# Performance work log

Hardware: AMD Instinct MI355X
Metric: run time of the kernel (lower is better)

Reference implementation:

```python
import jax, jax.numpy as jnp
import numpy as np

B, S = 2, 2048
NUM_HEADS, NUM_KV_HEADS, HEAD_DIM = 32, 8, 128
HIDDEN = NUM_HEADS * HEAD_DIM  # 4096
Q_SIZE = NUM_HEADS * HEAD_DIM
KV_SIZE = NUM_KV_HEADS * HEAD_DIM
ROPE_THETA = 100000.0
SCALE = HEAD_DIM ** -0.5


def setup_inputs() -> dict:
    key = jax.random.key(0)
    k1, k2, k3, k4, k5 = jax.random.split(key, 5)
    T = B * S
    return {
        "hidden_states": jax.random.normal(k1, (T, HIDDEN), jnp.float32) * 0.02,
        "positions": jnp.arange(T, dtype=jnp.int64) % S,  # per-sequence positions
        "w_qkv": jax.random.normal(k2, (HIDDEN, Q_SIZE + 2 * KV_SIZE), jnp.float32) * 0.02,
        "b_qkv": jax.random.normal(k3, (Q_SIZE + 2 * KV_SIZE,), jnp.float32) * 0.01,
        "w_o": jax.random.normal(k4, (Q_SIZE, HIDDEN), jnp.float32) * 0.02,
        "b_o": jax.random.normal(k5, (HIDDEN,), jnp.float32) * 0.01,
    }


def _rope_neox(x, positions):
    # x: [T, H, D]; neox style rotates the two halves of head_dim
    half = HEAD_DIM // 2
    inv_freq = 1.0 / (ROPE_THETA ** (jnp.arange(0, HEAD_DIM, 2, dtype=jnp.float32) / HEAD_DIM))
    freqs = positions.astype(jnp.float32)[:, None] * inv_freq[None, :]  # [T, D/2]
    cos = jnp.cos(freqs)[:, None, :]  # [T, 1, D/2]
    sin = jnp.sin(freqs)[:, None, :]
    x1, x2 = x[..., :half], x[..., half:]
    return jnp.concatenate([x1 * cos - x2 * sin, x2 * cos + x1 * sin], axis=-1)


def reference(hidden_states, positions, w_qkv, b_qkv, w_o, b_o):
    T = hidden_states.shape[0]
    qkv = hidden_states @ w_qkv + b_qkv  # [T, q+2kv]
    q = qkv[:, :Q_SIZE].reshape(T, NUM_HEADS, HEAD_DIM)
    k = qkv[:, Q_SIZE:Q_SIZE + KV_SIZE].reshape(T, NUM_KV_HEADS, HEAD_DIM)
    v = qkv[:, Q_SIZE + KV_SIZE:].reshape(T, NUM_KV_HEADS, HEAD_DIM)

    q = _rope_neox(q, positions)
    k = _rope_neox(k, positions)

    # reshape flattened tokens back to [B, S, ...] for causal self-attention
    q = q.reshape(B, S, NUM_HEADS, HEAD_DIM)
    k = k.reshape(B, S, NUM_KV_HEADS, HEAD_DIM)
    v = v.reshape(B, S, NUM_KV_HEADS, HEAD_DIM)

    # GQA: repeat kv heads to match query heads
    group = NUM_HEADS // NUM_KV_HEADS
    k = jnp.repeat(k, group, axis=2)  # [B, S, H, D]
    v = jnp.repeat(v, group, axis=2)

    scores = jnp.einsum("bqhd,bkhd->bhqk", q, k) * SCALE  # [B, H, S, S]
    causal = jnp.tril(jnp.ones((S, S), dtype=bool))
    scores = jnp.where(causal[None, None], scores, jnp.finfo(scores.dtype).min)
    probs = jax.nn.softmax(scores, axis=-1)
    attn = jnp.einsum("bhqk,bkhd->bqhd", probs, v)  # [B, S, H, D]

    attn = attn.reshape(T, Q_SIZE)
    return attn @ w_o + b_o  # [T, HIDDEN]
```

## Files before the change

### kernel.cpp

```cpp
#include <hip/hip_runtime.h>
#include <cstdint>
#include <math.h>

#define T_TOTAL 4096
#define S_LEN   2048
#define NH      32
#define NKV     8
#define HD      128
#define HIDDEN  4096
#define QSZ     4096
#define KVSZ    1024
#define QKV_N   6144
#define SCALE_F 0.08838834764831843f

typedef __bf16 bf16x8 __attribute__((ext_vector_type(8)));
typedef float  f32x4  __attribute__((ext_vector_type(4)));
typedef unsigned short u16;
typedef unsigned int   u32;
typedef u16 u16x8 __attribute__((ext_vector_type(8)));
typedef u16 u16x4 __attribute__((ext_vector_type(4)));

__device__ __forceinline__ u16 f2bf(float f) {
  u32 b = __float_as_uint(f);
  b += 0x7FFFu + ((b >> 16) & 1u);
  return (u16)(b >> 16);
}

__device__ __forceinline__ void async_copy16(const u16* g, u16* l) {
  __builtin_amdgcn_global_load_lds(
      (const __attribute__((address_space(1))) void*)(g),
      (__attribute__((address_space(3))) void*)(l), 16, 0, 0);
}

__global__ __launch_bounds__(256) void cast_bf16_kernel(const float4* __restrict__ in,
                                                        ushort4* __restrict__ out, int n4) {
  int i = blockIdx.x * 256 + threadIdx.x;
  if (i >= n4) return;
  float4 v = in[i];
  ushort4 o;
  o.x = f2bf(v.x); o.y = f2bf(v.y); o.z = f2bf(v.z); o.w = f2bf(v.w);
  out[i] = o;
}

__global__ __launch_bounds__(256) void transpose_cast_kernel(const float* __restrict__ in,
                                                             u16* __restrict__ out, int R, int C) {
  __shared__ float tile[32][33];
  int bx = blockIdx.x * 32;
  int by = blockIdx.y * 32;
  int tx = threadIdx.x & 31, ty = threadIdx.x >> 5;
  for (int i = ty; i < 32; i += 8)
    tile[i][tx] = in[(size_t)(by + i) * C + bx + tx];
  __syncthreads();
  for (int i = ty; i < 32; i += 8)
    out[(size_t)(bx + i) * R + by + tx] = f2bf(tile[tx][i]);
}

__global__ __launch_bounds__(256) void gemm_bt_kernel(const u16* __restrict__ A,
                                                      const u16* __restrict__ Bt,
                                                      const float* __restrict__ bias,
                                                      float* __restrict__ C,
                                                      int M, int N, int K) {
  __shared__ u16 sA[128 * 32];
  __shared__ u16 sB[128 * 32];
  const int tid  = threadIdx.x;
  const int lane = tid & 63, wave = tid >> 6;
  const int quad = lane >> 4, l16 = lane & 15;
  const int wm = (wave >> 1) * 64, wn = (wave & 1) * 64;
  const int bm = blockIdx.y, bn = blockIdx.x;

  const u16* gA0 = A  + (size_t)(bm * 128 + (tid >> 2)) * K + (tid & 3) * 8;
  const u16* gA1 = gA0 + (size_t)64 * K;
  const u16* gB0 = Bt + (size_t)(bn * 128 + (tid >> 2)) * K + (tid & 3) * 8;
  const u16* gB1 = gB0 + (size_t)64 * K;
  u16* lA0 = &sA[(size_t)tid * 8];
  u16* lA1 = &sA[(size_t)(256 + tid) * 8];
  u16* lB0 = &sB[(size_t)tid * 8];
  u16* lB1 = &sB[(size_t)(256 + tid) * 8];

  f32x4 acc[4][4] = {};

  for (int kt = 0; kt < K; kt += 32) {
    __syncthreads();
    async_copy16(gA0 + kt, lA0);
    async_copy16(gA1 + kt, lA1);
    async_copy16(gB0 + kt, lB0);
    async_copy16(gB1 + kt, lB1);
    __syncthreads();

    bf16x8 af[4], bfr[4];
#pragma unroll
    for (int i = 0; i < 4; ++i)
      af[i] = *(const bf16x8*)&sA[(wm + i * 16 + l16) * 32 + quad * 8];
#pragma unroll
    for (int j = 0; j < 4; ++j)
      bfr[j] = *(const bf16x8*)&sB[(wn + j * 16 + l16) * 32 + quad * 8];
#pragma unroll
    for (int i = 0; i < 4; ++i)
#pragma unroll
      for (int j = 0; j < 4; ++j)
        acc[i][j] = __builtin_amdgcn_mfma_f32_16x16x32_bf16(af[i], bfr[j], acc[i][j], 0, 0, 0);
  }

#pragma unroll
  for (int i = 0; i < 4; ++i) {
    int row0 = bm * 128 + wm + i * 16 + quad * 4;
#pragma unroll
    for (int j = 0; j < 4; ++j) {
      int col = bn * 128 + wn + j * 16 + l16;
      float bi = bias[col];
#pragma unroll
      for (int r = 0; r < 4; ++r)
        C[(size_t)(row0 + r) * N + col] = acc[i][j][r] + bi;
    }
  }
}

__global__ __launch_bounds__(256) void qk_rope_cast_kernel(const float* __restrict__ qkv,
                                                           const int* __restrict__ pos,
                                                           u16* __restrict__ Qb,
                                                           u16* __restrict__ Kb) {
  int idx = blockIdx.x * 256 + threadIdx.x;
  int t = idx / 2560;
  int rem = idx - t * 2560;
  int head = rem >> 6, i = rem & 63;
  int b = t >> 11, s = t & 2047;
  float p = (float)pos[t];
  float inv = exp2f(-(float)i * 0.25952563f);
  float f = p * inv;
  float sn, cs;
  sincosf(f, &sn, &cs);
  if (head < NH) {
    const float* src = qkv + (size_t)t * QKV_N + head * HD;
    float x1 = src[i], x2 = src[i + 64];
    u16* dst = Qb + (((size_t)(b * NH + head)) * S_LEN + s) * HD;
    dst[i]      = f2bf((x1 * cs - x2 * sn) * SCALE_F);
    dst[i + 64] = f2bf((x2 * cs + x1 * sn) * SCALE_F);
  } else {
    int kh = head - NH;
    const float* src = qkv + (size_t)t * QKV_N + QSZ + kh * HD;
    float x1 = src[i], x2 = src[i + 64];
    u16* dst = Kb + (((size_t)(b * NKV + kh)) * S_LEN + s) * HD;
    dst[i]      = f2bf(x1 * cs - x2 * sn);
    dst[i + 64] = f2bf(x2 * cs + x1 * sn);
  }
}

__global__ __launch_bounds__(256) void v_transpose_cast_kernel(const float* __restrict__ qkv,
                                                               u16* __restrict__ Vtb) {
  __shared__ float tile[32][33];
  int st = blockIdx.x * 32;
  int dt = blockIdx.y * 32;
  int bk = blockIdx.z;
  int b = bk >> 3, kvh = bk & 7;
  int tx = threadIdx.x & 31, ty = threadIdx.x >> 5;
  const float* src = qkv + (size_t)(b * S_LEN) * QKV_N + QSZ + KVSZ + kvh * HD;
  for (int i = ty; i < 32; i += 8)
    tile[i][tx] = src[(size_t)(st + i) * QKV_N + dt + tx];
  __syncthreads();
  u16* dst = Vtb + (size_t)bk * HD * S_LEN;
  for (int i = ty; i < 32; i += 8)
    dst[(size_t)(dt + i) * S_LEN + st + tx] = f2bf(tile[tx][i]);
}

__global__ __launch_bounds__(256) void flash_mfma_kernel(const u16* __restrict__ Qb,
                                                         const u16* __restrict__ Kb,
                                                         const u16* __restrict__ Vtb,
                                                         u16* __restrict__ attn) {
  const int qti = gridDim.x - 1 - blockIdx.x;
  const int h = blockIdx.y, b = blockIdx.z;
  const int kvh = h >> 2;
  const int tid = threadIdx.x;
  const int lane = tid & 63, wave = tid >> 6;
  const int quad = lane >> 4, l16 = lane & 15;

  __shared__ u16 sK[64 * 128];
  __shared__ u16 sVt[128 * 64];
  __shared__ u16 sP[4][16 * 64];

  bf16x8 qf[4];
  {
    const u16* qrow = Qb + (((size_t)(b * NH + h)) * S_LEN + (size_t)qti * 64 + wave * 16 + l16) * HD;
#pragma unroll
    for (int kc = 0; kc < 4; ++kc)
      qf[kc] = *(const bf16x8*)(qrow + kc * 32 + quad * 8);
  }

  f32x4 acc[8] = {};
  float m_r = -INFINITY;
  float l_r = 0.f;

  const u16* Kbase = Kb  + ((size_t)(b * NKV + kvh)) * S_LEN * HD;
  const u16* Vbase = Vtb + ((size_t)(b * NKV + kvh)) * HD * S_LEN;

  u16x8 kv[4], vv[4];
#pragma unroll
  for (int i = 0; i < 4; ++i) {
    int c = i * 256 + tid;
    kv[i] = *(const u16x8*)(Kbase + (size_t)(c >> 4) * HD + (c & 15) * 8);
    vv[i] = *(const u16x8*)(Vbase + (size_t)(c >> 3) * S_LEN + (c & 7) * 8);
  }

  for (int kt = 0; kt <= qti; ++kt) {
    __syncthreads();
#pragma unroll
    for (int i = 0; i < 4; ++i) {
      int c = i * 256 + tid;
      int kr = c >> 4;
      *(u16x8*)&sK[(kr * 128 + (c & 15) * 8) ^ ((kr & 7) << 3)] = kv[i];
      int vr = c >> 3;
      *(u16x8*)&sVt[(vr * 64 + (c & 7) * 8) ^ ((vr & 7) << 3)] = vv[i];
    }
    __syncthreads();

    if (kt < qti) {
#pragma unroll
      for (int i = 0; i < 4; ++i) {
        int c = i * 256 + tid;
        kv[i] = *(const u16x8*)(Kbase + (size_t)((kt + 1) * 64 + (c >> 4)) * HD + (c & 15) * 8);
        vv[i] = *(const u16x8*)(Vbase + (size_t)(c >> 3) * S_LEN + (kt + 1) * 64 + (c & 7) * 8);
      }
    }

    f32x4 s[4] = {};
#pragma unroll
    for (int kc = 0; kc < 4; ++kc) {
#pragma unroll
      for (int nb = 0; nb < 4; ++nb) {
        bf16x8 kf = *(const bf16x8*)&sK[((nb * 16 + l16) * 128 + kc * 32 + quad * 8) ^ ((l16 & 7) << 3)];
        s[nb] = __builtin_amdgcn_mfma_f32_16x16x32_bf16(kf, qf[kc], s[nb], 0, 0, 0);
      }
    }

    if (kt == qti) {
      int qloc = wave * 16 + l16;
#pragma unroll
      for (int nb = 0; nb < 4; ++nb)
#pragma unroll
        for (int r = 0; r < 4; ++r)
          if (nb * 16 + quad * 4 + r > qloc) s[nb][r] = -1e30f;
    }

    float mx = -1e30f;
#pragma unroll
    for (int nb = 0; nb < 4; ++nb)
#pragma unroll
      for (int r = 0; r < 4; ++r)
        mx = fmaxf(mx, s[nb][r]);
    mx = fmaxf(mx, __shfl_xor(mx, 16));
    mx = fmaxf(mx, __shfl_xor(mx, 32));
    float mnew = fmaxf(m_r, mx);
    float alpha = __expf(m_r - mnew);
    m_r = mnew;
    float rs = 0.f;
#pragma unroll
    for (int nb = 0; nb < 4; ++nb)
#pragma unroll
      for (int r = 0; r < 4; ++r) {
        float p = __expf(s[nb][r] - mnew);
        s[nb][r] = p;
        rs += p;
      }
    rs += __shfl_xor(rs, 16);
    rs += __shfl_xor(rs, 32);
    l_r = l_r * alpha + rs;

#pragma unroll
    for (int db = 0; db < 8; ++db)
#pragma unroll
      for (int r = 0; r < 4; ++r)
        acc[db][r] *= alpha;

    u16* sPw = sP[wave];
#pragma unroll
    for (int nb = 0; nb < 4; ++nb) {
      u16x4 pk;
#pragma unroll
      for (int r = 0; r < 4; ++r) pk[r] = f2bf(s[nb][r]);
      *(u16x4*)&sPw[(l16 * 64 + nb * 16 + quad * 4) ^ ((l16 & 7) << 3)] = pk;
    }

#pragma unroll
    for (int ch = 0; ch < 2; ++ch) {
      bf16x8 pf = *(const bf16x8*)&sPw[(l16 * 64 + ch * 32 + quad * 8) ^ ((l16 & 7) << 3)];
#pragma unroll
      for (int db = 0; db < 8; ++db) {
        bf16x8 vf = *(const bf16x8*)&sVt[((db * 16 + l16) * 64 + ch * 32 + quad * 8) ^ ((l16 & 7) << 3)];
        acc[db] = __builtin_amdgcn_mfma_f32_16x16x32_bf16(vf, pf, acc[db], 0, 0, 0);
      }
    }
  }

  float invl = 1.0f / l_r;
  __syncthreads();
  u16* sOw = &sK[wave * 2048];
#pragma unroll
  for (int db = 0; db < 8; ++db) {
    u16x4 pk;
#pragma unroll
    for (int r = 0; r < 4; ++r) pk[r] = f2bf(acc[db][r] * invl);
    *(u16x4*)&sOw[(l16 * 128 + db * 16 + quad * 4) ^ ((l16 & 7) << 3)] = pk;
  }
#pragma unroll
  for (int p = 0; p < 4; ++p) {
    int row = p * 4 + quad;
    u16x8 o = *(const u16x8*)&sOw[(row * 128 + l16 * 8) ^ ((row & 7) << 3)];
    int q = qti * 64 + wave * 16 + row;
    *(u16x8*)(attn + ((size_t)(b * S_LEN + q)) * QSZ + (size_t)h * HD + l16 * 8) = o;
  }
}

extern "C" void kernel_launch(void* const* d_in, const int* in_sizes, int n_in,
                              void* d_out, int out_size, void* d_ws, size_t ws_size,
                              hipStream_t stream) {
  const float* hidden    = (const float*)d_in[0];
  const int*   positions = (const int*)d_in[1];
  const float* w_qkv     = (const float*)d_in[2];
  const float* b_qkv     = (const float*)d_in[3];
  const float* w_o       = (const float*)d_in[4];
  const float* b_o       = (const float*)d_in[5];
  float* out = (float*)d_out;

  char* ws = (char*)d_ws;
  const size_t MB = 1024 * 1024;
  u16*   hb    = (u16*)ws;
  u16*   wqT   = (u16*)(ws + 32  * MB);
  u16*   woT   = (u16*)(ws + 80  * MB);
  float* qkv   = (float*)(ws + 112 * MB);
  u16*   attnb = (u16*)(ws + 208 * MB);
  u16*   Qb    = (u16*)ws;
  u16*   Kb    = (u16*)(ws + 32 * MB);
  u16*   Vtb   = (u16*)(ws + 40 * MB);

  cast_bf16_kernel<<<T_TOTAL * HIDDEN / 4 / 256, 256, 0, stream>>>(
      (const float4*)hidden, (ushort4*)hb, T_TOTAL * HIDDEN / 4);
  transpose_cast_kernel<<<dim3(QKV_N / 32, HIDDEN / 32), 256, 0, stream>>>(w_qkv, wqT, HIDDEN, QKV_N);
  transpose_cast_kernel<<<dim3(HIDDEN / 32, QSZ / 32), 256, 0, stream>>>(w_o, woT, QSZ, HIDDEN);
  gemm_bt_kernel<<<dim3(QKV_N / 128, T_TOTAL / 128), 256, 0, stream>>>(
      hb, wqT, b_qkv, qkv, T_TOTAL, QKV_N, HIDDEN);
  qk_rope_cast_kernel<<<T_TOTAL * 2560 / 256, 256, 0, stream>>>(qkv, positions, Qb, Kb);
  v_transpose_cast_kernel<<<dim3(S_LEN / 32, HD / 32, 16), 256, 0, stream>>>(qkv, Vtb);
  flash_mfma_kernel<<<dim3(S_LEN / 64, NH, 2), 256, 0, stream>>>(Qb, Kb, Vtb, attnb);
  gemm_bt_kernel<<<dim3(HIDDEN / 128, T_TOTAL / 128), 256, 0, stream>>>(
      attnb, woT, b_o, out, T_TOTAL, HIDDEN, QSZ);
}
```

Baseline: 1.020 ms.

## Replace GEMM with triple-buffered 256x256 tile kernel with swizzled LDS and XCD remap

Both projection GEMMs now use a new kernel with 512 threads and 256x256 output tiles. It keeps three stages of async global-to-LDS copies in flight with explicit vmcnt waits, so loads overlap the MFMA work. LDS columns are XOR-swizzled to cut bank conflicts, and block IDs are remapped across the 8 XCDs to improve L2 locality. The larger tiles and 3x32KB of LDS reduce occupancy, and fewer blocks (384 and 256) means less parallelism to fill the machine.

```diff
diff --git a/kernel.cpp b/kernel.cpp
--- a/kernel.cpp
+++ b/kernel.cpp
@@ -55,58 +55,82 @@
     out[(size_t)(bx + i) * R + by + tx] = f2bf(tile[tx][i]);
 }
 
-__global__ __launch_bounds__(256) void gemm_bt_kernel(const u16* __restrict__ A,
-                                                      const u16* __restrict__ Bt,
-                                                      const float* __restrict__ bias,
-                                                      float* __restrict__ C,
-                                                      int M, int N, int K) {
-  __shared__ u16 sA[128 * 32];
-  __shared__ u16 sB[128 * 32];
+__global__ __launch_bounds__(512) void gemm_pipe_kernel(const u16* __restrict__ A,
+                                                        const u16* __restrict__ Bt,
+                                                        const float* __restrict__ bias,
+                                                        float* __restrict__ C,
+                                                        int M, int N, int K, int nbn) {
+  __shared__ u16 lds[3][2][8192];
   const int tid  = threadIdx.x;
   const int lane = tid & 63, wave = tid >> 6;
   const int quad = lane >> 4, l16 = lane & 15;
-  const int wm = (wave >> 1) * 64, wn = (wave & 1) * 64;
-  const int bm = blockIdx.y, bn = blockIdx.x;
-
-  const u16* gA0 = A  + (size_t)(bm * 128 + (tid >> 2)) * K + (tid & 3) * 8;
-  const u16* gA1 = gA0 + (size_t)64 * K;
-  const u16* gB0 = Bt + (size_t)(bn * 128 + (tid >> 2)) * K + (tid & 3) * 8;
-  const u16* gB1 = gB0 + (size_t)64 * K;
-  u16* lA0 = &sA[(size_t)tid * 8];
-  u16* lA1 = &sA[(size_t)(256 + tid) * 8];
-  u16* lB0 = &sB[(size_t)tid * 8];
-  u16* lB1 = &sB[(size_t)(256 + tid) * 8];
-
-  f32x4 acc[4][4] = {};
-
-  for (int kt = 0; kt < K; kt += 32) {
-    __syncthreads();
-    async_copy16(gA0 + kt, lA0);
-    async_copy16(gA1 + kt, lA1);
-    async_copy16(gB0 + kt, lB0);
-    async_copy16(gB1 + kt, lB1);
-    __syncthreads();
-
-    bf16x8 af[4], bfr[4];
-#pragma unroll
-    for (int i = 0; i < 4; ++i)
-      af[i] = *(const bf16x8*)&sA[(wm + i * 16 + l16) * 32 + quad * 8];
+  const int wm = (wave >> 2) * 128;
+  const int wn = (wave & 3) * 64;
+
+  const int cpx = gridDim.x >> 3;
+  const int logical = (blockIdx.x & 7) * cpx + (blockIdx.x >> 3);
+  const int bm = logical / nbn, bn = logical % nbn;
+
+  const int trow = tid >> 2;
+  const int gch  = ((tid & 3) ^ ((tid >> 3) & 3)) * 8;
+  const u16* gA = A  + (size_t)(bm * 256 + trow) * K + gch;
+  const u16* gB = Bt + (size_t)(bn * 256 + trow) * K + gch;
+  const size_t eoff = (size_t)128 * K;
+
+  const int NT = K >> 5;
+#pragma unroll
+  for (int pt = 0; pt < 3; ++pt) {
+    int kt = pt * 32;
+    async_copy16(gA + kt,        &lds[pt][0][tid * 8]);
+    async_copy16(gA + eoff + kt, &lds[pt][0][4096 + tid * 8]);
+    async_copy16(gB + kt,        &lds[pt][1][tid * 8]);
+    async_copy16(gB + eoff + kt, &lds[pt][1][4096 + tid * 8]);
+  }
+
+  const int sw = (quad ^ ((l16 >> 1) & 3)) * 8;
+  f32x4 acc[8][4] = {};
+  int sl = 0;
+  for (int t = 0; t < NT; ++t) {
+    int rem = NT - t;
+    if (rem >= 3)      asm volatile("s_waitcnt vmcnt(8)" ::: "memory");
+    else if (rem == 2) asm volatile("s_waitcnt vmcnt(4)" ::: "memory");
+    else               asm volatile("s_waitcnt vmcnt(0)" ::: "memory");
+    __builtin_amdgcn_s_barrier();
+
+    const u16* sAt = lds[sl][0];
+    const u16* sBt = lds[sl][1];
+    bf16x8 af[8], bfr[4];
+#pragma unroll
+    for (int i = 0; i < 8; ++i)
+      af[i] = *(const bf16x8*)&sAt[(wm + i * 16 + l16) * 32 + sw];
 #pragma unroll
     for (int j = 0; j < 4; ++j)
-      bfr[j] = *(const bf16x8*)&sB[(wn + j * 16 + l16) * 32 + quad * 8];
-#pragma unroll
-    for (int i = 0; i < 4; ++i)
+      bfr[j] = *(const bf16x8*)&sBt[(wn + j * 16 + l16) * 32 + sw];
+    asm volatile("s_waitcnt lgkmcnt(0)" ::: "memory");
+    __builtin_amdgcn_s_barrier();
+
+    if (t + 3 < NT) {
+      int kt = (t + 3) * 32;
+      async_copy16(gA + kt,        &lds[sl][0][tid * 8]);
+      async_copy16(gA + eoff + kt, &lds[sl][0][4096 + tid * 8]);
+      async_copy16(gB + kt,        &lds[sl][1][tid * 8]);
+      async_copy16(gB + eoff + kt, &lds[sl][1][4096 + tid * 8]);
+    }
+
+#pragma unroll
+    for (int i = 0; i < 8; ++i)
 #pragma unroll
       for (int j = 0; j < 4; ++j)
         acc[i][j] = __builtin_amdgcn_mfma_f32_16x16x32_bf16(af[i], bfr[j], acc[i][j], 0, 0, 0);
-  }
-
-#pragma unroll
-  for (int i = 0; i < 4; ++i) {
-    int row0 = bm * 128 + wm + i * 16 + quad * 4;
+    sl = (sl == 2) ? 0 : sl + 1;
+  }
+
+#pragma unroll
+  for (int i = 0; i < 8; ++i) {
+    int row0 = bm * 256 + wm + i * 16 + quad * 4;
 #pragma unroll
     for (int j = 0; j < 4; ++j) {
-      int col = bn * 128 + wn + j * 16 + l16;
+      int col = bn * 256 + wn + j * 16 + l16;
       float bi = bias[col];
 #pragma unroll
       for (int r = 0; r < 4; ++r)
@@ -335,11 +359,11 @@
       (const float4*)hidden, (ushort4*)hb, T_TOTAL * HIDDEN / 4);
   transpose_cast_kernel<<<dim3(QKV_N / 32, HIDDEN / 32), 256, 0, stream>>>(w_qkv, wqT, HIDDEN, QKV_N);
   transpose_cast_kernel<<<dim3(HIDDEN / 32, QSZ / 32), 256, 0, stream>>>(w_o, woT, QSZ, HIDDEN);
-  gemm_bt_kernel<<<dim3(QKV_N / 128, T_TOTAL / 128), 256, 0, stream>>>(
-      hb, wqT, b_qkv, qkv, T_TOTAL, QKV_N, HIDDEN);
+  gemm_pipe_kernel<<<dim3((T_TOTAL / 256) * (QKV_N / 256)), 512, 0, stream>>>(
+      hb, wqT, b_qkv, qkv, T_TOTAL, QKV_N, HIDDEN, QKV_N / 256);
   qk_rope_cast_kernel<<<T_TOTAL * 2560 / 256, 256, 0, stream>>>(qkv, positions, Qb, Kb);
   v_transpose_cast_kernel<<<dim3(S_LEN / 32, HD / 32, 16), 256, 0, stream>>>(qkv, Vtb);
   flash_mfma_kernel<<<dim3(S_LEN / 64, NH, 2), 256, 0, stream>>>(Qb, Kb, Vtb, attnb);
-  gemm_bt_kernel<<<dim3(HIDDEN / 128, T_TOTAL / 128), 256, 0, stream>>>(
-      attnb, woT, b_o, out, T_TOTAL, HIDDEN, QSZ);
-}
+  gemm_pipe_kernel<<<dim3((T_TOTAL / 256) * (HIDDEN / 256)), 512, 0, stream>>>(
+      attnb, woT, b_o, out, T_TOTAL, HIDDEN, QSZ, HIDDEN / 256);
+}
```

Measured after the change: 922.2 us. 9.6% less time.
